# Performance work log

Measured on AMD Instinct MI355X. Metric: run time of the kernel, lower is better.

Reference implementation:

```python
import jax, jax.numpy as jnp
import numpy as np
import math

B, S, D, H = 4, 1024, 1024, 16
DK = D // H
LAT = (4, 4)


def _lattice_neighbors():
    # static 8-connectivity neighbor lists on the head lattice
    pos = [(i, j) for i in range(LAT[0]) for j in range(LAT[1])][:H]
    thresh = math.sqrt(2.0) + 0.1
    nbr_idx, nbr_dist = [], []
    for h, p in enumerate(pos):
        idx, dist = [], []
        for o, q in enumerate(pos):
            if o != h:
                d = math.sqrt((p[0] - q[0]) ** 2 + (p[1] - q[1]) ** 2)
                if d <= thresh:
                    idx.append(o)
                    dist.append(d)
        nbr_idx.append(np.asarray(idx, dtype=np.int32))
        nbr_dist.append(np.asarray(dist, dtype=np.float32))
    return nbr_idx, nbr_dist

NBR_IDX, NBR_DIST = _lattice_neighbors()


def setup_inputs() -> dict:
    rng = jax.random.key(0)
    ks = jax.random.split(rng, 8)
    bound = 1.0 / math.sqrt(D)  # torch Linear default init range
    return {
        "query": jax.random.normal(ks[0], (B, S, D), jnp.float32),
        "key": jax.random.normal(ks[1], (B, S, D), jnp.float32),
        "value": jax.random.normal(ks[2], (B, S, D), jnp.float32),
        "Wq": jax.random.uniform(ks[3], (H, DK, D), jnp.float32, -bound, bound),
        "Wk": jax.random.uniform(ks[4], (H, DK, D), jnp.float32, -bound, bound),
        "Wv": jax.random.uniform(ks[5], (H, DK, D), jnp.float32, -bound, bound),
        "intrinsic_freq": 1.0 + 0.1 * jnp.arange(H, dtype=jnp.float32),
        "phase": jnp.zeros((H,), jnp.float32),
        "lattice_coupling": 0.1 * jnp.ones((H,), jnp.float32),
        "lattice_constant": jnp.ones((H,), jnp.float32),
        "Wo": jax.random.uniform(ks[6], (D, D), jnp.float32, -bound, bound),
        "bo": jax.random.uniform(ks[7], (D,), jnp.float32, -bound, bound),
    }


def _update_phases(phase, intrinsic_freq, lattice_coupling, lattice_constant):
    # Sequential Kuramoto-style phase update: head h reads phases of lattice
    # neighbors (already-updated earlier heads included), matching the torch
    # per-head Python loop. The .data += update is not differentiated in
    # torch, hence stop_gradient on the delta.
    phases = phase
    for h in range(H):
        idx = NBR_IDX[h]
        if idx.size > 0:
            w = jnp.exp(-jnp.asarray(NBR_DIST[h]) / lattice_constant[h])
            force = jnp.sum(w * jnp.sin(phases[jnp.asarray(idx)] - phases[h]))
            cpl = lattice_coupling[h] * force
        else:
            cpl = jnp.float32(0.0)
        delta = 0.01 * (intrinsic_freq[h] + cpl)
        phases = phases.at[h].set(phases[h] + jax.lax.stop_gradient(delta))
    return phases


def reference(query, key, value, Wq, Wk, Wv, intrinsic_freq, phase,
              lattice_coupling, lattice_constant, Wo, bo):
    phases = _update_phases(phase, intrinsic_freq, lattice_coupling, lattice_constant)
    bias = 0.1 * jnp.cos(phases)  # [H] scalar additive bias per head

    Q = jnp.einsum('bsd,hed->bhse', query, Wq)  # [B,H,S,DK]
    K = jnp.einsum('btd,hed->bhte', key, Wk)
    V = jnp.einsum('btd,hed->bhte', value, Wv)

    scores = jnp.einsum('bhse,bhte->bhst', Q, K) / math.sqrt(DK)
    scores = scores + bias[None, :, None, None]
    attn = jax.nn.softmax(scores, axis=-1)  # [B,H,S,S]

    ctx = jnp.einsum('bhst,bhte->bhse', attn, V)  # [B,H,S,DK]
    concat = ctx.transpose(0, 2, 1, 3).reshape(B, S, D)  # head-order concat
    out = concat @ Wo.T + bo
    return out, attn
```

## Files before the change

kernel.cpp:

```cpp
#include <hip/hip_runtime.h>
#include <hip/hip_bf16.h>
#include <math.h>


typedef __bf16 bf16;
typedef __attribute__((ext_vector_type(8))) __bf16 bf16x8;
typedef __attribute__((ext_vector_type(4))) __bf16 bf16x4;
typedef __attribute__((ext_vector_type(4))) float f32x4;

#define MFMA16(a, b, c) __builtin_amdgcn_mfma_f32_16x16x32_bf16((a), (b), (c), 0, 0, 0)

__device__ __forceinline__ void gload_lds16(const void* g, void* l) {
  __builtin_amdgcn_global_load_lds(
      (const __attribute__((address_space(1))) unsigned int*)g,
      (__attribute__((address_space(3))) unsigned int*)l, 16, 0, 0);
}

__device__ __forceinline__ int swz(int col, int row) {
  return col ^ ((row & 7) << 3);
}

__device__ __forceinline__ void cvt_store8(const float* __restrict__ s,
                                           bf16* __restrict__ d) {
  const f32x4* sp = (const f32x4*)s;
  f32x4 a = sp[0], b = sp[1];
  bf16x8 o;
  o[0] = (bf16)a[0]; o[1] = (bf16)a[1]; o[2] = (bf16)a[2]; o[3] = (bf16)a[3];
  o[4] = (bf16)b[0]; o[5] = (bf16)b[1]; o[6] = (bf16)b[2]; o[7] = (bf16)b[3];
  *(bf16x8*)d = o;
}

__global__ __launch_bounds__(256) void k_cvt_all(
    const float* __restrict__ q, const float* __restrict__ k,
    const float* __restrict__ v, const float* __restrict__ wq,
    const float* __restrict__ wk, const float* __restrict__ wv,
    const float* __restrict__ wo, bf16* __restrict__ Xcat,
    bf16* __restrict__ Wqkv, bf16* __restrict__ Wob) {
  int bid = blockIdx.x;
  const float* src;
  bf16* dst;
  size_t loc;
  if (bid < 6144) {
    int which = bid >> 11;
    loc = (size_t)(bid & 2047) * 256 + threadIdx.x;
    src = which == 0 ? q : (which == 1 ? k : v);
    dst = Xcat + (size_t)which * 4194304;
  } else {
    bid -= 6144;
    int which = bid >> 9;
    loc = (size_t)(bid & 511) * 256 + threadIdx.x;
    src = which == 0 ? wq : (which == 1 ? wk : (which == 2 ? wv : wo));
    dst = which == 3 ? Wob : (Wqkv + (size_t)which * 1048576);
  }
  cvt_store8(src + loc * 8, dst + loc * 8);
}

__global__ __launch_bounds__(256) void k_gemm_qkv(const bf16* __restrict__ Xcat,
                                                  const bf16* __restrict__ Wqkv,
                                                  bf16* __restrict__ Qh,
                                                  bf16* __restrict__ Kh,
                                                  bf16* __restrict__ Vt) {
  const int orig = (blockIdx.x & 7) * 96 + (blockIdx.x >> 3);
  const int bx = orig & 7, by = orig >> 3;
  const int proj = by >> 5;
  const int mloc = by & 31;
  const bf16* Ab = Xcat + ((size_t)proj * 4096 + (size_t)mloc * 128) * 1024;
  const bf16* Bb = Wqkv + (size_t)proj * 1048576 + (size_t)bx * 128 * 1024;
  __shared__ alignas(16) char smem[34816];
  bf16* As = (bf16*)smem;
  bf16* Bs = (bf16*)(smem + 16384);
  const int tid = threadIdx.x, lane = tid & 63, wid = tid >> 6;
  const int q = lane & 15, quad = lane >> 4;
  const int wr = (wid >> 1) * 64, wc = (wid & 1) * 64;
  const int srow = tid >> 3, scol = (tid & 7) * 8;
  f32x4 acc[4][4] = {};
  for (int k0 = 0; k0 < 1024; k0 += 64) {
    __syncthreads();
#pragma unroll
    for (int p = 0; p < 4; ++p) {
      int r = srow + p * 32;
      int cg = k0 + swz(scol, r);
      gload_lds16(Ab + (size_t)r * 1024 + cg, &As[r * 64 + scol]);
      gload_lds16(Bb + (size_t)r * 1024 + cg, &Bs[r * 64 + scol]);
    }
    __syncthreads();
#pragma unroll
    for (int kk = 0; kk < 2; ++kk) {
      bf16x8 af[4], bfr[4];
#pragma unroll
      for (int m = 0; m < 4; ++m) {
        int row = wr + m * 16 + q;
        af[m] = *(const bf16x8*)&As[row * 64 + swz(kk * 32 + quad * 8, row)];
      }
#pragma unroll
      for (int n = 0; n < 4; ++n) {
        int row = wc + n * 16 + q;
        bfr[n] = *(const bf16x8*)&Bs[row * 64 + swz(kk * 32 + quad * 8, row)];
      }
#pragma unroll
      for (int m = 0; m < 4; ++m)
#pragma unroll
        for (int n = 0; n < 4; ++n) acc[m][n] = MFMA16(bfr[n], af[m], acc[m][n]);
    }
  }
  if (proj < 2) {
    bf16* dst = proj == 0 ? Qh : Kh;
#pragma unroll
    for (int m = 0; m < 4; ++m) {
      int grow = mloc * 128 + wr + m * 16 + q;
      int b = grow >> 10, s = grow & 1023;
#pragma unroll
      for (int n = 0; n < 4; ++n) {
        int col = bx * 128 + wc + n * 16 + quad * 4;
        int h = col >> 6, e = col & 63;
        bf16x4 o;
#pragma unroll
        for (int r = 0; r < 4; ++r) o[r] = (bf16)acc[m][n][r];
        *(bf16x4*)&dst[(((size_t)(b * 16 + h)) * 1024 + s) * 64 + e] = o;
      }
    }
  } else {
    __syncthreads();
    bf16* T = (bf16*)smem;
#pragma unroll
    for (int m = 0; m < 4; ++m) {
      int t_l = wr + m * 16 + q;
#pragma unroll
      for (int n = 0; n < 4; ++n) {
#pragma unroll
        for (int r = 0; r < 4; ++r) {
          int e_l = wc + n * 16 + quad * 4 + r;
          T[e_l * 136 + t_l] = (bf16)acc[m][n][r];
        }
      }
    }
    __syncthreads();
    const int b = mloc >> 3, t0 = (mloc & 7) * 128;
#pragma unroll
    for (int pass = 0; pass < 8; ++pass) {
      int e_l = pass * 16 + (tid >> 4);
      int toff = (tid & 15) * 8;
      bf16x8 vv = *(const bf16x8*)&T[e_l * 136 + toff];
      int eg = bx * 128 + e_l;
      int h = eg >> 6, e = eg & 63;
      *(bf16x8*)&Vt[(((size_t)(b * 16 + h) * 64 + e) * 1024) + t0 + toff] = vv;
    }
  }
}

__global__ __launch_bounds__(256) void k_gemm_out(const bf16* __restrict__ A,
                                                  const bf16* __restrict__ Bt,
                                                  const float* __restrict__ bo,
                                                  float* __restrict__ out) {
  const int orig = (blockIdx.x & 7) * 64 + (blockIdx.x >> 3);
  const int bx = orig & 15, by = orig >> 4;
  const bf16* Ab = A + (size_t)by * 128 * 1024;
  const bf16* Bb = Bt + (size_t)bx * 64 * 1024;
  __shared__ alignas(16) bf16 As[128 * 64];
  __shared__ alignas(16) bf16 Bs[64 * 64];
  const int tid = threadIdx.x, lane = tid & 63, wid = tid >> 6;
  const int q = lane & 15, quad = lane >> 4;
  const int wr = (wid >> 1) * 64, wc = (wid & 1) * 32;
  const int srow = tid >> 3, scol = (tid & 7) * 8;
  f32x4 acc[4][2] = {};
  for (int k0 = 0; k0 < 1024; k0 += 64) {
    __syncthreads();
#pragma unroll
    for (int p = 0; p < 4; ++p) {
      int r = srow + p * 32;
      int cg = k0 + swz(scol, r);
      gload_lds16(Ab + (size_t)r * 1024 + cg, &As[r * 64 + scol]);
      if (p < 2) gload_lds16(Bb + (size_t)r * 1024 + cg, &Bs[r * 64 + scol]);
    }
    __syncthreads();
#pragma unroll
    for (int kk = 0; kk < 2; ++kk) {
      bf16x8 af[4], bfr[2];
#pragma unroll
      for (int m = 0; m < 4; ++m) {
        int row = wr + m * 16 + q;
        af[m] = *(const bf16x8*)&As[row * 64 + swz(kk * 32 + quad * 8, row)];
      }
#pragma unroll
      for (int n = 0; n < 2; ++n) {
        int row = wc + n * 16 + q;
        bfr[n] = *(const bf16x8*)&Bs[row * 64 + swz(kk * 32 + quad * 8, row)];
      }
#pragma unroll
      for (int m = 0; m < 4; ++m)
#pragma unroll
        for (int n = 0; n < 2; ++n) acc[m][n] = MFMA16(bfr[n], af[m], acc[m][n]);
    }
  }
#pragma unroll
  for (int m = 0; m < 4; ++m) {
    int row = by * 128 + wr + m * 16 + q;
#pragma unroll
    for (int n = 0; n < 2; ++n) {
      int colg = bx * 64 + wc + n * 16 + quad * 4;
      f32x4 o = acc[m][n] + *(const f32x4*)&bo[colg];
      *(f32x4*)&out[(size_t)row * 1024 + colg] = o;
    }
  }
}

#define PLD 1032
__global__ __launch_bounds__(512) void k_scores_pv(
    const bf16* __restrict__ Qh, const bf16* __restrict__ Kh,
    const bf16* __restrict__ Vt, float* __restrict__ attn,
    bf16* __restrict__ concat) {
  const int bid = blockIdx.x;
  const int xcd = bid & 7, idx = bid >> 3;
  const int bh = xcd * 8 + (idx & 7);
  const int chunk0 = (idx >> 3) * 4;
  const int b = bh >> 4, h = bh & 15;
  const int tid = threadIdx.x, lane = tid & 63, wid = tid >> 6;
  const int q = lane & 15, quad = lane >> 4;
  __shared__ alignas(16) bf16 P_lds[32 * PLD];
  __shared__ float red[8][32];

  const bf16* Kb = Kh + (size_t)bh * 65536;

  for (int s = 0; s < 4; ++s) {
    const int row0 = (chunk0 + s) * 32;
    const bf16* Qb = Qh + ((size_t)bh * 1024 + row0) * 64;
    bf16x8 qfA0 = *(const bf16x8*)&Qb[q * 64 + quad * 8];
    bf16x8 qfA1 = *(const bf16x8*)&Qb[q * 64 + 32 + quad * 8];
    bf16x8 qfB0 = *(const bf16x8*)&Qb[(16 + q) * 64 + quad * 8];
    bf16x8 qfB1 = *(const bf16x8*)&Qb[(16 + q) * 64 + 32 + quad * 8];

    float lsA = 0.f, lsB = 0.f;
#pragma unroll 4
    for (int n = 0; n < 8; ++n) {
      const int kr = wid * 128 + n * 16 + q;
      const bf16* kp = &Kb[(size_t)kr * 64 + quad * 8];
      bf16x8 kf0 = *(const bf16x8*)kp;
      bf16x8 kf1 = *(const bf16x8*)(kp + 32);
      f32x4 cA = {0.f, 0.f, 0.f, 0.f}, cB = {0.f, 0.f, 0.f, 0.f};
      __builtin_amdgcn_s_setprio(1);
      cA = MFMA16(kf0, qfA0, cA);
      cA = MFMA16(kf1, qfA1, cA);
      cB = MFMA16(kf0, qfB0, cB);
      cB = MFMA16(kf1, qfB1, cB);
      __builtin_amdgcn_s_setprio(0);
      bf16x4 pbA, pbB;
#pragma unroll
      for (int r = 0; r < 4; ++r) {
        float pA = __expf(cA[r] * 0.125f);
        float pB = __expf(cB[r] * 0.125f);
        lsA += pA; lsB += pB;
        pbA[r] = (bf16)pA; pbB[r] = (bf16)pB;
      }
      int tcol = wid * 128 + n * 16 + quad * 4;
      *(bf16x4*)&P_lds[q * PLD + tcol] = pbA;
      *(bf16x4*)&P_lds[(16 + q) * PLD + tcol] = pbB;
    }
    lsA += __shfl_xor(lsA, 16); lsA += __shfl_xor(lsA, 32);
    lsB += __shfl_xor(lsB, 16); lsB += __shfl_xor(lsB, 32);
    if (lane < 16) {
      red[wid][lane] = lsA;
      red[wid][16 + lane] = lsB;
    }
    __syncthreads();

#pragma unroll
    for (int i = 0; i < 4; ++i) {
      int row = wid * 4 + i;
      float sm = red[0][row] + red[1][row] + red[2][row] + red[3][row] +
                 red[4][row] + red[5][row] + red[6][row] + red[7][row];
      float invi = 1.f / sm;
      float* abase = attn + ((size_t)bh * 1024 + row0 + row) * 1024;
#pragma unroll
      for (int c = 0; c < 4; ++c) {
        bf16x4 p4 = *(const bf16x4*)&P_lds[row * PLD + c * 256 + lane * 4];
        f32x4 v;
        v[0] = (float)p4[0] * invi; v[1] = (float)p4[1] * invi;
        v[2] = (float)p4[2] * invi; v[3] = (float)p4[3] * invi;
        __builtin_nontemporal_store(v, (f32x4*)(abase + c * 256 + lane * 4));
      }
    }

    const int qg = wid >> 2, es = wid & 3;
    const bf16* vptr = Vt + ((size_t)bh * 64 + es * 16 + q) * 1024 + quad * 8;
    const bf16* pptr = &P_lds[(qg * 16 + q) * PLD + quad * 8];
    f32x4 c0 = {0.f, 0.f, 0.f, 0.f}, c1 = {0.f, 0.f, 0.f, 0.f};
    __builtin_amdgcn_s_setprio(1);
#pragma unroll
    for (int k0 = 0; k0 < 1024; k0 += 64) {
      c0 = MFMA16(*(const bf16x8*)(vptr + k0), *(const bf16x8*)(pptr + k0), c0);
      c1 = MFMA16(*(const bf16x8*)(vptr + k0 + 32), *(const bf16x8*)(pptr + k0 + 32), c1);
    }
    __builtin_amdgcn_s_setprio(0);
    int prow = qg * 16 + q;
    float sm = red[0][prow] + red[1][prow] + red[2][prow] + red[3][prow] +
               red[4][prow] + red[5][prow] + red[6][prow] + red[7][prow];
    f32x4 cc = (c0 + c1) * (1.f / sm);
    bf16x4 ob;
#pragma unroll
    for (int r = 0; r < 4; ++r) ob[r] = (bf16)cc[r];
    *(bf16x4*)&concat[((size_t)(b * 1024 + row0 + prow)) * 1024 + h * 64 +
                      es * 16 + quad * 4] = ob;
    __syncthreads();
  }
}

extern "C" void kernel_launch(void* const* d_in, const int* in_sizes, int n_in,
                              void* d_out, int out_size, void* d_ws, size_t ws_size,
                              hipStream_t stream) {
  const float* query = (const float*)d_in[0];
  const float* key   = (const float*)d_in[1];
  const float* value = (const float*)d_in[2];
  const float* Wq    = (const float*)d_in[3];
  const float* Wk    = (const float*)d_in[4];
  const float* Wv    = (const float*)d_in[5];
  const float* Wo    = (const float*)d_in[10];
  const float* bo    = (const float*)d_in[11];

  float* out  = (float*)d_out;
  float* attn = out + (size_t)4 * 1024 * 1024;

  bf16* Xcat = (bf16*)d_ws;
  bf16* Wqkv = Xcat + (size_t)12288 * 1024;
  bf16* Wobf = Wqkv + (size_t)3 * 1024 * 1024;
  bf16* Qhb  = Wobf + (size_t)1024 * 1024;
  bf16* Khb  = Qhb + (size_t)64 * 1024 * 64;
  bf16* Vt   = Khb + (size_t)64 * 1024 * 64;
  bf16* Conc = Vt + (size_t)64 * 64 * 1024;

  k_cvt_all<<<8192, 256, 0, stream>>>(query, key, value, Wq, Wk, Wv, Wo,
                                      Xcat, Wqkv, Wobf);
  k_gemm_qkv<<<768, 256, 0, stream>>>(Xcat, Wqkv, Qhb, Khb, Vt);
  k_scores_pv<<<512, 512, 0, stream>>>(Qhb, Khb, Vt, attn, Conc);
  k_gemm_out<<<512, 256, 0, stream>>>(Conc, Wobf, bo, out);
}
```

Baseline: 152.8 us.

## Fuse activation fp32-to-bf16 conversion into QKV GEMM tile loads

The separate conversion pass over query/key/value is removed. The QKV GEMM now loads fp32 activation tiles straight into LDS with a swizzled layout and converts them to bf16 while reading MFMA fragments. Only the weights still go through a standalone conversion kernel. This avoids writing and re-reading a 24MB bf16 activation copy, at the cost of twice the LDS footprint for A tiles, twice the global A traffic per tile (re-read by the 8 column blocks), and conversion work in the inner loop.

```diff
diff --git a/kernel.cpp b/kernel.cpp
--- a/kernel.cpp
+++ b/kernel.cpp
@@ -20,42 +20,28 @@
   return col ^ ((row & 7) << 3);
 }
 
-__device__ __forceinline__ void cvt_store8(const float* __restrict__ s,
-                                           bf16* __restrict__ d) {
-  const f32x4* sp = (const f32x4*)s;
-  f32x4 a = sp[0], b = sp[1];
+__device__ __forceinline__ bf16x8 cvt8(f32x4 a, f32x4 b) {
   bf16x8 o;
   o[0] = (bf16)a[0]; o[1] = (bf16)a[1]; o[2] = (bf16)a[2]; o[3] = (bf16)a[3];
   o[4] = (bf16)b[0]; o[5] = (bf16)b[1]; o[6] = (bf16)b[2]; o[7] = (bf16)b[3];
-  *(bf16x8*)d = o;
-}
-
-__global__ __launch_bounds__(256) void k_cvt_all(
-    const float* __restrict__ q, const float* __restrict__ k,
-    const float* __restrict__ v, const float* __restrict__ wq,
-    const float* __restrict__ wk, const float* __restrict__ wv,
-    const float* __restrict__ wo, bf16* __restrict__ Xcat,
+  return o;
+}
+
+__global__ __launch_bounds__(256) void k_cvtw(
+    const float* __restrict__ wq, const float* __restrict__ wk,
+    const float* __restrict__ wv, const float* __restrict__ wo,
     bf16* __restrict__ Wqkv, bf16* __restrict__ Wob) {
-  int bid = blockIdx.x;
-  const float* src;
-  bf16* dst;
-  size_t loc;
-  if (bid < 6144) {
-    int which = bid >> 11;
-    loc = (size_t)(bid & 2047) * 256 + threadIdx.x;
-    src = which == 0 ? q : (which == 1 ? k : v);
-    dst = Xcat + (size_t)which * 4194304;
-  } else {
-    bid -= 6144;
-    int which = bid >> 9;
-    loc = (size_t)(bid & 511) * 256 + threadIdx.x;
-    src = which == 0 ? wq : (which == 1 ? wk : (which == 2 ? wv : wo));
-    dst = which == 3 ? Wob : (Wqkv + (size_t)which * 1048576);
-  }
-  cvt_store8(src + loc * 8, dst + loc * 8);
-}
-
-__global__ __launch_bounds__(256) void k_gemm_qkv(const bf16* __restrict__ Xcat,
+  int which = blockIdx.x >> 9;
+  size_t loc = (size_t)(blockIdx.x & 511) * 256 + threadIdx.x;
+  const float* src = which == 0 ? wq : (which == 1 ? wk : (which == 2 ? wv : wo));
+  bf16* dst = which == 3 ? Wob : (Wqkv + (size_t)which * 1048576);
+  const f32x4* sp = (const f32x4*)(src + loc * 8);
+  *(bf16x8*)(dst + loc * 8) = cvt8(sp[0], sp[1]);
+}
+
+__global__ __launch_bounds__(256) void k_gemm_qkv(const float* __restrict__ qf,
+                                                  const float* __restrict__ kf,
+                                                  const float* __restrict__ vf,
                                                   const bf16* __restrict__ Wqkv,
                                                   bf16* __restrict__ Qh,
                                                   bf16* __restrict__ Kh,
@@ -64,24 +50,31 @@
   const int bx = orig & 7, by = orig >> 3;
   const int proj = by >> 5;
   const int mloc = by & 31;
-  const bf16* Ab = Xcat + ((size_t)proj * 4096 + (size_t)mloc * 128) * 1024;
+  const float* Af = (proj == 0 ? qf : (proj == 1 ? kf : vf)) +
+                    (size_t)mloc * 128 * 1024;
   const bf16* Bb = Wqkv + (size_t)proj * 1048576 + (size_t)bx * 128 * 1024;
-  __shared__ alignas(16) char smem[34816];
-  bf16* As = (bf16*)smem;
-  bf16* Bs = (bf16*)(smem + 16384);
+  __shared__ alignas(16) char smem[49152];
+  float* Asf = (float*)smem;
+  bf16* Bs = (bf16*)(smem + 32768);
   const int tid = threadIdx.x, lane = tid & 63, wid = tid >> 6;
   const int q = lane & 15, quad = lane >> 4;
   const int wr = (wid >> 1) * 64, wc = (wid & 1) * 64;
-  const int srow = tid >> 3, scol = (tid & 7) * 8;
+  const int srowB = tid >> 3, scolB = (tid & 7) * 8;
+  const int rowA0 = tid >> 4, g16 = tid & 15;
+  const int agrp = g16 >> 1, ahalf = (g16 & 1) * 4;
   f32x4 acc[4][4] = {};
   for (int k0 = 0; k0 < 1024; k0 += 64) {
     __syncthreads();
 #pragma unroll
     for (int p = 0; p < 4; ++p) {
-      int r = srow + p * 32;
-      int cg = k0 + swz(scol, r);
-      gload_lds16(Ab + (size_t)r * 1024 + cg, &As[r * 64 + scol]);
-      gload_lds16(Bb + (size_t)r * 1024 + cg, &Bs[r * 64 + scol]);
+      int r = srowB + p * 32;
+      gload_lds16(Bb + (size_t)r * 1024 + k0 + swz(scolB, r), &Bs[r * 64 + scolB]);
+    }
+#pragma unroll
+    for (int p = 0; p < 8; ++p) {
+      int r = rowA0 + p * 16;
+      int srccol = ((agrp ^ (r & 7)) << 3) + ahalf;
+      gload_lds16(Af + (size_t)r * 1024 + k0 + srccol, &Asf[r * 64 + g16 * 4]);
     }
     __syncthreads();
 #pragma unroll
@@ -90,7 +83,9 @@
 #pragma unroll
       for (int m = 0; m < 4; ++m) {
         int row = wr + m * 16 + q;
-        af[m] = *(const bf16x8*)&As[row * 64 + swz(kk * 32 + quad * 8, row)];
+        int grp = (kk * 4 + quad) ^ (row & 7);
+        const f32x4* ap = (const f32x4*)&Asf[row * 64 + grp * 8];
+        af[m] = cvt8(ap[0], ap[1]);
       }
 #pragma unroll
       for (int n = 0; n < 4; ++n) {
@@ -319,17 +314,15 @@
   float* out  = (float*)d_out;
   float* attn = out + (size_t)4 * 1024 * 1024;
 
-  bf16* Xcat = (bf16*)d_ws;
-  bf16* Wqkv = Xcat + (size_t)12288 * 1024;
+  bf16* Wqkv = (bf16*)d_ws;
   bf16* Wobf = Wqkv + (size_t)3 * 1024 * 1024;
   bf16* Qhb  = Wobf + (size_t)1024 * 1024;
   bf16* Khb  = Qhb + (size_t)64 * 1024 * 64;
   bf16* Vt   = Khb + (size_t)64 * 1024 * 64;
   bf16* Conc = Vt + (size_t)64 * 64 * 1024;
 
-  k_cvt_all<<<8192, 256, 0, stream>>>(query, key, value, Wq, Wk, Wv, Wo,
-                                      Xcat, Wqkv, Wobf);
-  k_gemm_qkv<<<768, 256, 0, stream>>>(Xcat, Wqkv, Qhb, Khb, Vt);
+  k_cvtw<<<2048, 256, 0, stream>>>(Wq, Wk, Wv, Wo, Wqkv, Wobf);
+  k_gemm_qkv<<<768, 256, 0, stream>>>(query, key, value, Wqkv, Qhb, Khb, Vt);
   k_scores_pv<<<512, 512, 0, stream>>>(Qhb, Khb, Vt, attn, Conc);
   k_gemm_out<<<512, 256, 0, stream>>>(Conc, Wobf, bo, out);
 }
```

Measured after the change: 168.0 us. +10.0%, slower.
